# Kernel tuning notes

Measured on AMD Instinct MI355X. Metric: run time of the kernel, lower is better.

Reference implementation:

```python
import jax, jax.numpy as jnp
import numpy as np

D_ENC, D_PRED, D_JOINT, VOCAB = 512, 640, 640, 1024

def setup_inputs() -> dict:
    key = jax.random.key(0)
    ks = jax.random.split(key, 8)
    B, T, U = 8, 200, 50
    s_enc = 1.0 / np.sqrt(D_ENC)
    s_pred = 1.0 / np.sqrt(D_PRED)
    s_joint = 1.0 / np.sqrt(D_JOINT)
    return {
        "encoder_out": jax.random.normal(ks[0], (B, T, D_ENC), jnp.float32),
        "predictor_out": jax.random.normal(ks[1], (B, U, D_PRED), jnp.float32),
        # nn.Linear weights: (out, in), uniform(-1/sqrt(in), 1/sqrt(in))
        "W_enc": jax.random.uniform(ks[2], (D_JOINT, D_ENC), jnp.float32, -s_enc, s_enc),
        "b_enc": jax.random.uniform(ks[3], (D_JOINT,), jnp.float32, -s_enc, s_enc),
        "W_pred": jax.random.uniform(ks[4], (D_JOINT, D_PRED), jnp.float32, -s_pred, s_pred),
        "b_pred": jax.random.uniform(ks[5], (D_JOINT,), jnp.float32, -s_pred, s_pred),
        "W_out": jax.random.uniform(ks[6], (VOCAB, D_JOINT), jnp.float32, -s_joint, s_joint),
        "b_out": jax.random.uniform(ks[7], (VOCAB,), jnp.float32, -s_joint, s_joint),
    }

def reference(encoder_out, predictor_out, W_enc, b_enc, W_pred, b_pred, W_out, b_out):
    # (B,T,d_joint) and (B,U,d_joint) projections
    enc = jnp.einsum('btd,jd->btj', encoder_out, W_enc) + b_enc
    pred = jnp.einsum('bud,jd->buj', predictor_out, W_pred) + b_pred
    # broadcast-add over (T,U), tanh, then output projection -> (B,T,U,V)
    joint = jnp.tanh(enc[:, :, None, :] + pred[:, None, :, :])
    return jnp.einsum('btuj,vj->btuv', joint, W_out) + b_out
```

## Files before the change

kernel.cpp:

```cpp
#include <hip/hip_runtime.h>
#include <hip/hip_bf16.h>
#include <stdint.h>
#include <stddef.h>

#define D_ENC 512
#define D_J   640
#define VOCAB 1024
#define BB    8
#define TT    200
#define UU    50

typedef __bf16 bf16x8 __attribute__((ext_vector_type(8)));
typedef float  f32x4  __attribute__((ext_vector_type(4)));

static __device__ __forceinline__ unsigned f2bf(float x) {
    union { float f; unsigned u; } v; v.f = x;
    unsigned r = v.u + 0x7FFFu + ((v.u >> 16) & 1u);
    return r >> 16;
}
static __device__ __forceinline__ unsigned pk2(float a, float b) {
    return f2bf(a) | (f2bf(b) << 16);
}

static __device__ __forceinline__ float tanh_fast(float x) {
    float ax = __builtin_fabsf(x);
    float e  = __expf(-2.0f * ax);
    float t  = (1.0f - e) * __builtin_amdgcn_rcpf(1.0f + e);
    return __builtin_copysignf(t, x);
}

__global__ void wcvt_kernel(const float* __restrict__ src,
                            unsigned short* __restrict__ dst, int n8) {
    int i = blockIdx.x * blockDim.x + threadIdx.x;
    if (i >= n8) return;
    const float4* s = (const float4*)src + (size_t)i * 2;
    float4 a = s[0], b = s[1];
    uint4 o;
    o.x = pk2(a.x, a.y); o.y = pk2(a.z, a.w);
    o.z = pk2(b.x, b.y); o.w = pk2(b.z, b.w);
    ((uint4*)dst)[i] = o;
}

__global__ void proj_gemm(const float* __restrict__ A, const float* __restrict__ W,
                          const float* __restrict__ bias, float* __restrict__ C,
                          int M, int K) {
    __shared__ __align__(16) unsigned short Alds[64 * 72];
    __shared__ __align__(16) unsigned short Blds[64 * 72];
    const int tid  = threadIdx.x;
    const int lane = tid & 63, w = tid >> 6;
    const int l15  = lane & 15, quad = lane >> 4;
    const int m0 = blockIdx.x * 64, n0 = blockIdx.y * 64;
    const int srow = tid >> 2, sq = tid & 3;

    f32x4 acc[4];
#pragma unroll
    for (int i = 0; i < 4; ++i) acc[i] = (f32x4){0.f, 0.f, 0.f, 0.f};

    const int am = m0 + srow;
    const float* arow = A + (size_t)am * K + sq * 16;
    const float* wrow = W + (size_t)(n0 + srow) * K + sq * 16;
    unsigned short* adst = &Alds[srow * 72 + sq * 16];
    unsigned short* bdst = &Blds[srow * 72 + sq * 16];

    for (int k0 = 0; k0 < K; k0 += 64) {
        uint4 wa0, wa1;
        if (am < M) {
            const float4* p = (const float4*)(arow + k0);
            float4 x0 = p[0], x1 = p[1], x2 = p[2], x3 = p[3];
            wa0.x = pk2(x0.x, x0.y); wa0.y = pk2(x0.z, x0.w);
            wa0.z = pk2(x1.x, x1.y); wa0.w = pk2(x1.z, x1.w);
            wa1.x = pk2(x2.x, x2.y); wa1.y = pk2(x2.z, x2.w);
            wa1.z = pk2(x3.x, x3.y); wa1.w = pk2(x3.z, x3.w);
        } else {
            wa0 = make_uint4(0u, 0u, 0u, 0u); wa1 = wa0;
        }
        uint4 wb0, wb1;
        {
            const float4* p = (const float4*)(wrow + k0);
            float4 x0 = p[0], x1 = p[1], x2 = p[2], x3 = p[3];
            wb0.x = pk2(x0.x, x0.y); wb0.y = pk2(x0.z, x0.w);
            wb0.z = pk2(x1.x, x1.y); wb0.w = pk2(x1.z, x1.w);
            wb1.x = pk2(x2.x, x2.y); wb1.y = pk2(x2.z, x2.w);
            wb1.z = pk2(x3.x, x3.y); wb1.w = pk2(x3.z, x3.w);
        }
        *(uint4*)adst = wa0; *(uint4*)(adst + 8) = wa1;
        *(uint4*)bdst = wb0; *(uint4*)(bdst + 8) = wb1;
        __syncthreads();
#pragma unroll
        for (int ks = 0; ks < 2; ++ks) {
            bf16x8 af = *(const bf16x8*)&Alds[(w * 16 + l15) * 72 + ks * 32 + quad * 8];
#pragma unroll
            for (int nt = 0; nt < 4; ++nt) {
                bf16x8 bf = *(const bf16x8*)&Blds[(nt * 16 + l15) * 72 + ks * 32 + quad * 8];
                acc[nt] = __builtin_amdgcn_mfma_f32_16x16x32_bf16(af, bf, acc[nt], 0, 0, 0);
            }
        }
        __syncthreads();
    }
#pragma unroll
    for (int nt = 0; nt < 4; ++nt) {
        const int n = n0 + nt * 16 + l15;
        const float bo = bias[n];
#pragma unroll
        for (int r = 0; r < 4; ++r) {
            const int mm = m0 + w * 16 + quad * 4 + r;
            if (mm < M) C[(size_t)mm * D_J + n] = acc[nt][r] + bo;
        }
    }
}

#define TANH4(d, e, p)                         \
    d.x = tanh_fast(e.x + p.x);                \
    d.y = tanh_fast(e.y + p.y);                \
    d.z = tanh_fast(e.z + p.z);                \
    d.w = tanh_fast(e.w + p.w);

__global__ void joint_kernel(const float* __restrict__ encp,
                             const float* __restrict__ predp,
                             const unsigned short* __restrict__ Wb,
                             const float* __restrict__ bout,
                             float* __restrict__ out) {
    __shared__ __align__(16) unsigned short Alds[64 * 72];
    const int tid  = threadIdx.x;
    const int lane = tid & 63, w = tid >> 6;
    const int l15  = lane & 15, quad = lane >> 4;
    const int m0 = blockIdx.x * 64;
    const int n0 = blockIdx.y * 256 + w * 64;
    const int srow = tid >> 2, sq = tid & 3;

    const int m  = m0 + srow;
    const int bt = m / UU;
    const int u  = m - bt * UU;
    const int b  = bt / TT;
    const float* erow = encp  + (size_t)bt * D_J + sq * 16;
    const float* prow = predp + (size_t)(b * UU + u) * D_J + sq * 16;
    const unsigned short* wrow = Wb + (size_t)(n0 + l15) * D_J + quad * 8;
    unsigned short* adst = &Alds[srow * 72 + sq * 16];

    f32x4 acc[4][4];
#pragma unroll
    for (int i = 0; i < 4; ++i)
#pragma unroll
        for (int j = 0; j < 4; ++j) acc[i][j] = (f32x4){0.f, 0.f, 0.f, 0.f};

    for (int k0 = 0; k0 < D_J; k0 += 64) {
        uint4 bfr[2][4];
#pragma unroll
        for (int ks = 0; ks < 2; ++ks)
#pragma unroll
            for (int nt = 0; nt < 4; ++nt)
                bfr[ks][nt] = *(const uint4*)(wrow + (size_t)nt * 16 * D_J + k0 + ks * 32);

        {
            const float4* ep = (const float4*)(erow + k0);
            const float4* pp = (const float4*)(prow + k0);
            float4 e0 = ep[0], e1 = ep[1], e2 = ep[2], e3 = ep[3];
            float4 p0 = pp[0], p1 = pp[1], p2 = pp[2], p3 = pp[3];
            float4 t0, t1, t2, t3;
            TANH4(t0, e0, p0); TANH4(t1, e1, p1);
            TANH4(t2, e2, p2); TANH4(t3, e3, p3);
            uint4 s0, s1;
            s0.x = pk2(t0.x, t0.y); s0.y = pk2(t0.z, t0.w);
            s0.z = pk2(t1.x, t1.y); s0.w = pk2(t1.z, t1.w);
            s1.x = pk2(t2.x, t2.y); s1.y = pk2(t2.z, t2.w);
            s1.z = pk2(t3.x, t3.y); s1.w = pk2(t3.z, t3.w);
            *(uint4*)adst = s0;
            *(uint4*)(adst + 8) = s1;
        }
        __syncthreads();
#pragma unroll
        for (int ks = 0; ks < 2; ++ks) {
            bf16x8 af[4];
#pragma unroll
            for (int mt = 0; mt < 4; ++mt)
                af[mt] = *(const bf16x8*)&Alds[(mt * 16 + l15) * 72 + ks * 32 + quad * 8];
#pragma unroll
            for (int mt = 0; mt < 4; ++mt)
#pragma unroll
                for (int nt = 0; nt < 4; ++nt)
                    acc[mt][nt] = __builtin_amdgcn_mfma_f32_16x16x32_bf16(
                        af[mt], __builtin_bit_cast(bf16x8, bfr[ks][nt]), acc[mt][nt], 0, 0, 0);
        }
        __syncthreads();
    }

#pragma unroll
    for (int nt = 0; nt < 4; ++nt) {
        const int n = n0 + nt * 16 + l15;
        const float bo = bout[n];
#pragma unroll
        for (int mt = 0; mt < 4; ++mt) {
#pragma unroll
            for (int r = 0; r < 4; ++r) {
                const int mm = m0 + mt * 16 + quad * 4 + r;
                out[(size_t)mm * VOCAB + n] = acc[mt][nt][r] + bo;
            }
        }
    }
}

extern "C" void kernel_launch(void* const* d_in, const int* in_sizes, int n_in,
                              void* d_out, int out_size, void* d_ws, size_t ws_size,
                              hipStream_t stream) {
    const float* enc    = (const float*)d_in[0];
    const float* pred   = (const float*)d_in[1];
    const float* W_enc  = (const float*)d_in[2];
    const float* b_enc  = (const float*)d_in[3];
    const float* W_pred = (const float*)d_in[4];
    const float* b_pred = (const float*)d_in[5];
    const float* W_out  = (const float*)d_in[6];
    const float* b_out  = (const float*)d_in[7];
    float* out = (float*)d_out;

    char* ws = (char*)d_ws;
    unsigned short* Wob = (unsigned short*)ws;
    float* encp  = (float*)(ws + 1310720);
    float* predp = (float*)(ws + 1310720 + 4096000);

    wcvt_kernel<<<320, 256, 0, stream>>>(W_out, Wob, 81920);
    proj_gemm<<<dim3(25, 10), 256, 0, stream>>>(enc,  W_enc,  b_enc,  encp,  1600, 512);
    proj_gemm<<<dim3(7, 10),  256, 0, stream>>>(pred, W_pred, b_pred, predp, 400,  640);
    joint_kernel<<<dim3(1250, 4), 256, 0, stream>>>(encp, predp, Wob, b_out, out);
}
```

Measured before the change: 630.5 us.

## Compute tanh A-tile once per row block across full vocab with double-buffered LDS

The joint kernel now uses 512-thread blocks of 8 waves, each covering 128 vocab columns, so one block spans all 1024 outputs for its 64 rows. This removes the 4x redundant tanh/bf16 staging of the A tile that happened when the vocab was split across grid.y. The A tile is double-buffered in LDS, so the next k-step is staged while the MFMAs run, and one barrier per iteration is dropped. In exchange each wave holds a 4x8 accumulator array (128 floats), which raises register pressure, and the launch bound of 2 blocks per CU may limit occupancy.

```diff
diff --git a/kernel.cpp b/kernel.cpp
--- a/kernel.cpp
+++ b/kernel.cpp
@@ -115,77 +115,80 @@
     d.z = tanh_fast(e.z + p.z);                \
     d.w = tanh_fast(e.w + p.w);
 
-__global__ void joint_kernel(const float* __restrict__ encp,
-                             const float* __restrict__ predp,
-                             const unsigned short* __restrict__ Wb,
-                             const float* __restrict__ bout,
-                             float* __restrict__ out) {
-    __shared__ __align__(16) unsigned short Alds[64 * 72];
+#define STAGE(dstp, kk)                                      \
+    {                                                        \
+        const float4* ep = (const float4*)(erow + (kk));     \
+        const float4* pp = (const float4*)(prow + (kk));     \
+        float4 e0 = ep[0], e1 = ep[1];                       \
+        float4 p0 = pp[0], p1 = pp[1];                       \
+        float4 t0, t1;                                       \
+        TANH4(t0, e0, p0); TANH4(t1, e1, p1);                \
+        uint4 s;                                             \
+        s.x = pk2(t0.x, t0.y); s.y = pk2(t0.z, t0.w);        \
+        s.z = pk2(t1.x, t1.y); s.w = pk2(t1.z, t1.w);        \
+        *(uint4*)(dstp) = s;                                 \
+    }
+
+__global__ void __launch_bounds__(512, 2)
+joint_kernel(const float* __restrict__ encp,
+             const float* __restrict__ predp,
+             const unsigned short* __restrict__ Wb,
+             const float* __restrict__ bout,
+             float* __restrict__ out) {
+    __shared__ __align__(16) unsigned short Alds[2][64 * 72];
     const int tid  = threadIdx.x;
     const int lane = tid & 63, w = tid >> 6;
-    const int l15  = lane & 15, quad = lane >> 4;
+    const int l15  = lane & 15, quad = (lane >> 4) & 3;
     const int m0 = blockIdx.x * 64;
-    const int n0 = blockIdx.y * 256 + w * 64;
-    const int srow = tid >> 2, sq = tid & 3;
+    const int n0 = w * 128;
+    const int srow = tid >> 3, sq = tid & 7;
 
     const int m  = m0 + srow;
     const int bt = m / UU;
     const int u  = m - bt * UU;
     const int b  = bt / TT;
-    const float* erow = encp  + (size_t)bt * D_J + sq * 16;
-    const float* prow = predp + (size_t)(b * UU + u) * D_J + sq * 16;
+    const float* erow = encp  + (size_t)bt * D_J + sq * 8;
+    const float* prow = predp + (size_t)(b * UU + u) * D_J + sq * 8;
     const unsigned short* wrow = Wb + (size_t)(n0 + l15) * D_J + quad * 8;
-    unsigned short* adst = &Alds[srow * 72 + sq * 16];
-
-    f32x4 acc[4][4];
+    unsigned short* adst0 = &Alds[0][srow * 72 + sq * 8];
+    unsigned short* adst1 = adst0 + 64 * 72;
+
+    f32x4 acc[4][8];
 #pragma unroll
     for (int i = 0; i < 4; ++i)
 #pragma unroll
-        for (int j = 0; j < 4; ++j) acc[i][j] = (f32x4){0.f, 0.f, 0.f, 0.f};
-
-    for (int k0 = 0; k0 < D_J; k0 += 64) {
-        uint4 bfr[2][4];
-#pragma unroll
-        for (int ks = 0; ks < 2; ++ks)
-#pragma unroll
-            for (int nt = 0; nt < 4; ++nt)
-                bfr[ks][nt] = *(const uint4*)(wrow + (size_t)nt * 16 * D_J + k0 + ks * 32);
-
-        {
-            const float4* ep = (const float4*)(erow + k0);
-            const float4* pp = (const float4*)(prow + k0);
-            float4 e0 = ep[0], e1 = ep[1], e2 = ep[2], e3 = ep[3];
-            float4 p0 = pp[0], p1 = pp[1], p2 = pp[2], p3 = pp[3];
-            float4 t0, t1, t2, t3;
-            TANH4(t0, e0, p0); TANH4(t1, e1, p1);
-            TANH4(t2, e2, p2); TANH4(t3, e3, p3);
-            uint4 s0, s1;
-            s0.x = pk2(t0.x, t0.y); s0.y = pk2(t0.z, t0.w);
-            s0.z = pk2(t1.x, t1.y); s0.w = pk2(t1.z, t1.w);
-            s1.x = pk2(t2.x, t2.y); s1.y = pk2(t2.z, t2.w);
-            s1.z = pk2(t3.x, t3.y); s1.w = pk2(t3.z, t3.w);
-            *(uint4*)adst = s0;
-            *(uint4*)(adst + 8) = s1;
+        for (int j = 0; j < 8; ++j) acc[i][j] = (f32x4){0.f, 0.f, 0.f, 0.f};
+
+    STAGE(adst0, 0);
+    __syncthreads();
+
+    for (int kt = 0; kt < 10; ++kt) {
+        const int k0  = kt * 64;
+        const int cur = kt & 1;
+        if (kt < 9) STAGE(cur ? adst0 : adst1, k0 + 64);
+
+#pragma unroll
+        for (int ks = 0; ks < 2; ++ks) {
+            uint4 bfr[8];
+#pragma unroll
+            for (int nt = 0; nt < 8; ++nt)
+                bfr[nt] = *(const uint4*)(wrow + (size_t)nt * 16 * D_J + k0 + ks * 32);
+            bf16x8 af[4];
+#pragma unroll
+            for (int mt = 0; mt < 4; ++mt)
+                af[mt] = *(const bf16x8*)&Alds[cur][(mt * 16 + l15) * 72 + ks * 32 + quad * 8];
+#pragma unroll
+            for (int mt = 0; mt < 4; ++mt)
+#pragma unroll
+                for (int nt = 0; nt < 8; ++nt)
+                    acc[mt][nt] = __builtin_amdgcn_mfma_f32_16x16x32_bf16(
+                        af[mt], __builtin_bit_cast(bf16x8, bfr[nt]), acc[mt][nt], 0, 0, 0);
         }
         __syncthreads();
-#pragma unroll
-        for (int ks = 0; ks < 2; ++ks) {
-            bf16x8 af[4];
-#pragma unroll
-            for (int mt = 0; mt < 4; ++mt)
-                af[mt] = *(const bf16x8*)&Alds[(mt * 16 + l15) * 72 + ks * 32 + quad * 8];
-#pragma unroll
-            for (int mt = 0; mt < 4; ++mt)
-#pragma unroll
-                for (int nt = 0; nt < 4; ++nt)
-                    acc[mt][nt] = __builtin_amdgcn_mfma_f32_16x16x32_bf16(
-                        af[mt], __builtin_bit_cast(bf16x8, bfr[ks][nt]), acc[mt][nt], 0, 0, 0);
-        }
-        __syncthreads();
-    }
-
-#pragma unroll
-    for (int nt = 0; nt < 4; ++nt) {
+    }
+
+#pragma unroll
+    for (int nt = 0; nt < 8; ++nt) {
         const int n = n0 + nt * 16 + l15;
         const float bo = bout[n];
 #pragma unroll
@@ -220,5 +223,5 @@
     wcvt_kernel<<<320, 256, 0, stream>>>(W_out, Wob, 81920);
     proj_gemm<<<dim3(25, 10), 256, 0, stream>>>(enc,  W_enc,  b_enc,  encp,  1600, 512);
     proj_gemm<<<dim3(7, 10),  256, 0, stream>>>(pred, W_pred, b_pred, predp, 400,  640);
-    joint_kernel<<<dim3(1250, 4), 256, 0, stream>>>(encp, predp, Wob, b_out, out);
-}
+    joint_kernel<<<dim3(1250), 512, 0, stream>>>(encp, predp, Wob, b_out, out);
+}
```

After: 607.7 us. 3.6% less time.
